# Kernel tuning notes

Measured on AMD Instinct MI355X. Metric: run time of the kernel, lower is better.

Reference implementation:

```python
import jax, jax.numpy as jnp
import numpy as np

NUM_HEADS = 16
HEAD_DIM = 64
HIDDEN = NUM_HEADS * HEAD_DIM
LN_EPS = 1e-6


def setup_inputs() -> dict:
    key = jax.random.key(0)
    ks = jax.random.split(key, 5)
    B, T, H = 2, 2048, HIDDEN
    s = 1.0 / np.sqrt(H)
    return {
        "h": jax.random.normal(ks[0], (B, T, H), jnp.float32),
        "Wq": jax.random.normal(ks[1], (H, H), jnp.float32) * s,
        "bq": jnp.zeros((H,), jnp.float32),
        "Wk": jax.random.normal(ks[2], (H, H), jnp.float32) * s,
        "bk": jnp.zeros((H,), jnp.float32),
        "Wv": jax.random.normal(ks[3], (H, H), jnp.float32) * s,
        "bv": jnp.zeros((H,), jnp.float32),
        "Wo": jax.random.normal(ks[4], (H, H), jnp.float32) * s,
        "bo": jnp.zeros((H,), jnp.float32),
        "gamma": jnp.ones((H,), jnp.float32),
        "beta": jnp.zeros((H,), jnp.float32),
    }


def _split_heads(x):
    B, T, H = x.shape
    return x.reshape(B, T, NUM_HEADS, HEAD_DIM).transpose(0, 2, 1, 3)  # [B,h,T,d]


def reference(h, Wq, bq, Wk, bk, Wv, bv, Wo, bo, gamma, beta):
    # QKV projections (nn.Linear: x @ W^T + b)
    Q = _split_heads(h @ Wq.T + bq)
    K = _split_heads(h @ Wk.T + bk)
    V = _split_heads(h @ Wv.T + bv)
    scale = HEAD_DIM ** -0.5
    scores = jnp.einsum("bhqd,bhkd->bhqk", Q, K) * scale  # [B,h,T,T]
    attn = jax.nn.softmax(scores, axis=-1)
    ctx = jnp.einsum("bhqk,bhkd->bhqd", attn, V)          # [B,h,T,d]
    B, _, T, _ = ctx.shape
    ctx = ctx.transpose(0, 2, 1, 3).reshape(B, T, HIDDEN)
    out = ctx @ Wo.T + bo + h  # dropout is identity at eval
    # LayerNorm(eps=1e-6)
    mu = out.mean(-1, keepdims=True)
    var = jnp.mean((out - mu) ** 2, -1, keepdims=True)
    return (out - mu) * jax.lax.rsqrt(var + LN_EPS) * gamma + beta
```

## Files before the change

### kernel.cpp

```cpp
#include <hip/hip_runtime.h>
#include <hip/hip_bf16.h>

#define NH   16
#define HD   64
#define HID  1024
#define TSEQ 2048
#define BATCH 2
#define KSCALE 0.18033688011112042f

typedef __attribute__((ext_vector_type(4))) float f32x4;
typedef __attribute__((ext_vector_type(8))) short s16x8;
typedef __attribute__((ext_vector_type(4))) short s16x4;
typedef __attribute__((ext_vector_type(8))) _Float16 f16x8;
typedef __attribute__((ext_vector_type(4))) _Float16 f16x4;
typedef __attribute__((ext_vector_type(2))) _Float16 f16x2;

__device__ __forceinline__ unsigned short f2bf(float f) {
  union { float f; unsigned int u; } v; v.f = f;
  unsigned int r = v.u + 0x7fffu + ((v.u >> 16) & 1u);
  return (unsigned short)(r >> 16);
}
__device__ __forceinline__ float bf2f(unsigned short b) {
  union { unsigned int u; float f; } v; v.u = ((unsigned int)b) << 16; return v.f;
}

__device__ __forceinline__ void async_cp16(const unsigned short* g, unsigned short* l) {
  __builtin_amdgcn_global_load_lds(
      (const __attribute__((address_space(1))) unsigned int*)g,
      (__attribute__((address_space(3))) unsigned int*)l, 16, 0, 0);
}

__global__ __launch_bounds__(256) void cast_all_k(
    const float* __restrict__ h,
    const float* __restrict__ w0, const float* __restrict__ w1,
    const float* __restrict__ w2, const float* __restrict__ w3,
    unsigned short* __restrict__ hb, unsigned short* __restrict__ wbase) {
  int i = blockIdx.x * 256 + threadIdx.x;
  const float* src; unsigned short* dst; int idx; float sc = 1.f;
  if (i < 1048576) { src = h; dst = hb; idx = i; }
  else {
    int idx4 = i - 1048576;
    int w = idx4 >> 18;
    idx = idx4 & 262143;
    src = (w == 0) ? w0 : (w == 1) ? w1 : (w == 2) ? w2 : w3;
    dst = wbase + (size_t)(idx4 - idx) * 4;
    if (w == 1) sc = KSCALE;
  }
  float4 v = ((const float4*)src)[idx];
  ushort4 o;
  o.x = f2bf(v.x * sc); o.y = f2bf(v.y * sc); o.z = f2bf(v.z * sc); o.w = f2bf(v.w * sc);
  ((ushort4*)dst)[idx] = o;
}

__global__ __launch_bounds__(256) void gemm_qkv(
    const unsigned short* __restrict__ hb,
    const unsigned short* __restrict__ wq, const unsigned short* __restrict__ wk,
    const unsigned short* __restrict__ wv,
    const float* __restrict__ bq, const float* __restrict__ bk, const float* __restrict__ bv,
    unsigned short* __restrict__ qo, unsigned short* __restrict__ ko,
    unsigned short* __restrict__ vto) {
  __shared__ unsigned short Ash[64 * 32];
  __shared__ unsigned short Bsh[3][64 * 32];
  const int tid = threadIdx.x, lane = tid & 63, wave = tid >> 6;
  const int l15 = lane & 15, quad = lane >> 4;
  const int wn = wave * 16;
  const int bm = blockIdx.y * 64, bn = blockIdx.x * 64;
  const unsigned short* Ag = hb + (size_t)bm * HID;
  const unsigned short* Bg0 = wq + (size_t)bn * HID;
  const unsigned short* Bg1 = wk + (size_t)bn * HID;
  const unsigned short* Bg2 = wv + (size_t)bn * HID;
  const int idx = tid * 8;
  const int rA = idx >> 5, cA = idx & 31;

  f32x4 acc[3][4];
#pragma unroll
  for (int m = 0; m < 3; ++m)
#pragma unroll
    for (int i = 0; i < 4; ++i) acc[m][i] = f32x4{0.f, 0.f, 0.f, 0.f};

  for (int k0 = 0; k0 < HID; k0 += 32) {
    __syncthreads();
    async_cp16(Ag  + rA * HID + k0 + cA, Ash    + idx);
    async_cp16(Bg0 + rA * HID + k0 + cA, Bsh[0] + idx);
    async_cp16(Bg1 + rA * HID + k0 + cA, Bsh[1] + idx);
    async_cp16(Bg2 + rA * HID + k0 + cA, Bsh[2] + idx);
    __syncthreads();
    s16x8 af[4];
#pragma unroll
    for (int i = 0; i < 4; ++i)
      af[i] = *(const s16x8*)(Ash + (i * 16 + l15) * 32 + quad * 8);
#pragma unroll
    for (int m = 0; m < 3; ++m) {
      s16x8 bfr = *(const s16x8*)(Bsh[m] + (wn + l15) * 32 + quad * 8);
#pragma unroll
      for (int i = 0; i < 4; ++i)
        acc[m][i] = __builtin_amdgcn_mfma_f32_16x16x32_bf16(af[i], bfr, acc[m][i], 0, 0, 0);
    }
  }

  const int col = bn + wn + l15;
  const int head = col >> 6, d = col & 63;
  {
    const float bb = bq[col];
#pragma unroll
    for (int i = 0; i < 4; ++i) {
#pragma unroll
      for (int r = 0; r < 4; ++r) {
        const int row = bm + i * 16 + quad * 4 + r;
        const int bI = row >> 11, t = row & 2047;
        qo[(((size_t)(bI * NH + head) * TSEQ) + t) * HD + d] = f2bf(acc[0][i][r] + bb);
      }
    }
  }
  {
    const float bb = bk[col] * KSCALE;
#pragma unroll
    for (int i = 0; i < 4; ++i) {
#pragma unroll
      for (int r = 0; r < 4; ++r) {
        const int row = bm + i * 16 + quad * 4 + r;
        const int bI = row >> 11, t = row & 2047;
        ko[(((size_t)(bI * NH + head) * TSEQ) + t) * HD + d] = f2bf(acc[1][i][r] + bb);
      }
    }
  }
  {
    const float bb = bv[col];
#pragma unroll
    for (int i = 0; i < 4; ++i) {
      const int row0 = bm + i * 16 + quad * 4;
      const int bI = row0 >> 11, t0 = row0 & 2047;
      unsigned short o[4];
#pragma unroll
      for (int r = 0; r < 4; ++r) {
        _Float16 hv = (_Float16)(acc[2][i][r] + bb);
        o[r] = __builtin_bit_cast(unsigned short, hv);
      }
      *(s16x4*)(vto + ((size_t)((bI * NH + head) * HD + d)) * TSEQ + t0) = *(const s16x4*)o;
    }
  }
}

__global__ __launch_bounds__(256) void gemm_out(
    const unsigned short* __restrict__ ctx, const unsigned short* __restrict__ wo,
    const float* __restrict__ bo, const float* __restrict__ hres,
    float* __restrict__ outf) {
  __shared__ unsigned short Ash[128 * 32];
  __shared__ unsigned short Bsh[64 * 32];
  const int tid = threadIdx.x, lane = tid & 63, wave = tid >> 6;
  const int l15 = lane & 15, quad = lane >> 4;
  const int wm = (wave >> 1) * 64, wn = (wave & 1) * 32;
  const int bm = blockIdx.y * 128, bn = blockIdx.x * 64;
  const unsigned short* Ag = ctx + (size_t)bm * HID;
  const unsigned short* Bg = wo + (size_t)bn * HID;
  const int idx0 = tid * 8, idx1 = idx0 + 2048;
  const int r0 = idx0 >> 5, c0 = idx0 & 31;
  const int r1 = idx1 >> 5, c1 = idx1 & 31;
  f32x4 acc[4][2];
#pragma unroll
  for (int i = 0; i < 4; ++i)
#pragma unroll
    for (int j = 0; j < 2; ++j) acc[i][j] = f32x4{0.f, 0.f, 0.f, 0.f};

  for (int k0 = 0; k0 < HID; k0 += 32) {
    __syncthreads();
    async_cp16(Ag + r0 * HID + k0 + c0, Ash + idx0);
    async_cp16(Ag + r1 * HID + k0 + c1, Ash + idx1);
    async_cp16(Bg + r0 * HID + k0 + c0, Bsh + idx0);
    __syncthreads();
    s16x8 af[4], bfr[2];
#pragma unroll
    for (int i = 0; i < 4; ++i)
      af[i] = *(const s16x8*)(Ash + (wm + i * 16 + l15) * 32 + quad * 8);
#pragma unroll
    for (int j = 0; j < 2; ++j)
      bfr[j] = *(const s16x8*)(Bsh + (wn + j * 16 + l15) * 32 + quad * 8);
#pragma unroll
    for (int i = 0; i < 4; ++i)
#pragma unroll
      for (int j = 0; j < 2; ++j)
        acc[i][j] = __builtin_amdgcn_mfma_f32_16x16x32_bf16(af[i], bfr[j], acc[i][j], 0, 0, 0);
  }
#pragma unroll
  for (int j = 0; j < 2; ++j) {
    const int col = bn + wn + j * 16 + l15;
    const float bb = bo[col];
#pragma unroll
    for (int i = 0; i < 4; ++i) {
#pragma unroll
      for (int r = 0; r < 4; ++r) {
        const int row = bm + wm + i * 16 + quad * 4 + r;
        const size_t off = (size_t)row * HID + col;
        outf[off] = acc[i][j][r] + bb + hres[off];
      }
    }
  }
}

__global__ __launch_bounds__(256, 2) void attn_k(
    const unsigned short* __restrict__ qb, const unsigned short* __restrict__ kb,
    const unsigned short* __restrict__ vt, unsigned short* __restrict__ ctx,
    unsigned short* __restrict__ Opart, float* __restrict__ rsumP,
    int lsplit, int ntiles) {
  __shared__ unsigned short Ksh[64 * 72];
  __shared__ unsigned short Vsh[64 * 72];

  const int tid = threadIdx.x, lane = tid & 63, wave = tid >> 6;
  const int l15 = lane & 15, quad = lane >> 4;
  const int z = blockIdx.z;
  const int b = z >> lsplit;
  const int part = z & ((1 << lsplit) - 1);
  const int h = blockIdx.y, qt = blockIdx.x;
  const size_t ho = ((size_t)(b * NH + h)) * TSEQ * HD;
  const unsigned short* Qh = qb + ho;
  const unsigned short* Kh = kb + ho;
  const unsigned short* Vh = vt + ho;
  const int q0 = qt * 128 + wave * 32;
  const int kt0 = part * ntiles;

  s16x8 qf[2][2];
#pragma unroll
  for (int s = 0; s < 2; ++s)
#pragma unroll
    for (int ks = 0; ks < 2; ++ks)
      qf[s][ks] = *(const s16x8*)(Qh + (size_t)(q0 + s * 16 + l15) * HD + ks * 32 + quad * 8);

  f32x4 accO[4][2];
  float rsum[2];
#pragma unroll
  for (int n2 = 0; n2 < 4; ++n2)
#pragma unroll
    for (int s = 0; s < 2; ++s) accO[n2][s] = f32x4{0.f, 0.f, 0.f, 0.f};
  rsum[0] = rsum[1] = 0.f;

  const int sr = tid >> 3, sc = (tid & 7) * 8;
  s16x8 kreg[2], vreg[2];
#pragma unroll
  for (int hf = 0; hf < 2; ++hf) {
    kreg[hf] = *(const s16x8*)(Kh + (size_t)(kt0 * 64 + sr + hf * 32) * HD + sc);
    vreg[hf] = *(const s16x8*)(Vh + (size_t)(sr + hf * 32) * TSEQ + kt0 * 64 + sc);
  }

  for (int kt = 0; kt < ntiles; ++kt) {
    __syncthreads();
#pragma unroll
    for (int hf = 0; hf < 2; ++hf) {
      *(s16x8*)(Ksh + (sr + hf * 32) * 72 + sc) = kreg[hf];
      *(s16x8*)(Vsh + (sr + hf * 32) * 72 + sc) = vreg[hf];
    }
    __syncthreads();
    if (kt + 1 < ntiles) {
      const int k0n = (kt0 + kt + 1) * 64;
#pragma unroll
      for (int hf = 0; hf < 2; ++hf) {
        kreg[hf] = *(const s16x8*)(Kh + (size_t)(k0n + sr + hf * 32) * HD + sc);
        vreg[hf] = *(const s16x8*)(Vh + (size_t)(sr + hf * 32) * TSEQ + k0n + sc);
      }
    }

    f32x4 accS[2][4];
#pragma unroll
    for (int s = 0; s < 2; ++s)
#pragma unroll
      for (int n = 0; n < 4; ++n) accS[s][n] = f32x4{0.f, 0.f, 0.f, 0.f};
#pragma unroll
    for (int ks = 0; ks < 2; ++ks) {
#pragma unroll
      for (int n = 0; n < 4; ++n) {
        s16x8 kf = *(const s16x8*)(Ksh + (n * 16 + l15) * 72 + ks * 32 + quad * 8);
#pragma unroll
        for (int s = 0; s < 2; ++s)
          accS[s][n] = __builtin_amdgcn_mfma_f32_16x16x32_bf16(kf, qf[s][ks], accS[s][n], 0, 0, 0);
      }
    }

    f16x4 pB[2][4];
#pragma unroll
    for (int s = 0; s < 2; ++s)
#pragma unroll
      for (int n = 0; n < 4; ++n) {
        float e0 = __builtin_amdgcn_exp2f(accS[s][n][0]);
        float e1 = __builtin_amdgcn_exp2f(accS[s][n][1]);
        float e2 = __builtin_amdgcn_exp2f(accS[s][n][2]);
        float e3 = __builtin_amdgcn_exp2f(accS[s][n][3]);
        rsum[s] += (e0 + e1) + (e2 + e3);
        f16x2 lo = __builtin_bit_cast(f16x2, __builtin_amdgcn_cvt_pkrtz(e0, e1));
        f16x2 hi = __builtin_bit_cast(f16x2, __builtin_amdgcn_cvt_pkrtz(e2, e3));
        pB[s][n] = f16x4{lo[0], lo[1], hi[0], hi[1]};
      }

#pragma unroll
    for (int n = 0; n < 4; ++n) {
#pragma unroll
      for (int n2 = 0; n2 < 4; ++n2) {
        f16x4 vA = *(const f16x4*)(Vsh + (n2 * 16 + l15) * 72 + n * 16 + quad * 4);
#pragma unroll
        for (int s = 0; s < 2; ++s)
          accO[n2][s] = __builtin_amdgcn_mfma_f32_16x16x16f16(vA, pB[s][n], accO[n2][s], 0, 0, 0);
      }
    }
  }

#pragma unroll
  for (int s = 0; s < 2; ++s) {
    float t = rsum[s];
    t += __shfl_xor(t, 16, 64);
    t += __shfl_xor(t, 32, 64);
    rsum[s] = t;
  }

  if (lsplit) {
    const int slot = (part * BATCH + b) * NH + h;
    const size_t ob = (size_t)slot * TSEQ * HD;
#pragma unroll
    for (int s = 0; s < 2; ++s) {
      const int t = q0 + s * 16 + l15;
#pragma unroll
      for (int n2 = 0; n2 < 4; ++n2) {
        const int d0 = n2 * 16 + quad * 4;
        unsigned short o[4];
#pragma unroll
        for (int r = 0; r < 4; ++r) o[r] = f2bf(accO[n2][s][r]);
        *(s16x4*)(Opart + ob + (size_t)t * HD + d0) = *(const s16x4*)o;
      }
    }
    if (quad == 0) {
      const size_t rb = (size_t)slot * TSEQ;
#pragma unroll
      for (int s = 0; s < 2; ++s)
        rsumP[rb + q0 + s * 16 + l15] = rsum[s];
    }
  } else {
#pragma unroll
    for (int s = 0; s < 2; ++s) {
      const int t = q0 + s * 16 + l15;
      const float inv = 1.f / rsum[s];
#pragma unroll
      for (int n2 = 0; n2 < 4; ++n2) {
        const int d0 = n2 * 16 + quad * 4;
        unsigned short o[4];
#pragma unroll
        for (int r = 0; r < 4; ++r) o[r] = f2bf(accO[n2][s][r] * inv);
        *(s16x4*)(ctx + ((size_t)(b * TSEQ + t)) * HID + h * HD + d0) = *(const s16x4*)o;
      }
    }
  }
}

__global__ __launch_bounds__(256) void combine_k(
    const unsigned short* __restrict__ Opart, const float* __restrict__ rsumP,
    unsigned short* __restrict__ ctx, int nparts) {
  const int gtid = blockIdx.x * 256 + threadIdx.x;
  const int d = (gtid & 7) * 8;
  const int rem = gtid >> 3;
  const int t = rem & 2047;
  const int bh = rem >> 11;
  float acc[8] = {0, 0, 0, 0, 0, 0, 0, 0};
  float rs = 0.f;
  for (int p = 0; p < nparts; ++p) {
    const int slot = p * 32 + bh;
    s16x8 a = *(const s16x8*)(Opart + ((size_t)slot * TSEQ + t) * HD + d);
#pragma unroll
    for (int j = 0; j < 8; ++j) acc[j] += bf2f(((const unsigned short*)&a)[j]);
    rs += rsumP[(size_t)slot * TSEQ + t];
  }
  const float inv = 1.f / rs;
  unsigned short o[8];
#pragma unroll
  for (int j = 0; j < 8; ++j) o[j] = f2bf(acc[j] * inv);
  const int b = bh >> 4, h = bh & 15;
  *(s16x8*)(ctx + ((size_t)(b * TSEQ + t)) * HID + h * HD + d) = *(const s16x8*)o;
}

__global__ __launch_bounds__(256) void ln_k(float* __restrict__ io,
                                            const float* __restrict__ gamma,
                                            const float* __restrict__ beta) {
  const int row = blockIdx.x, tid = threadIdx.x;
  float x[4]; float s = 0.f, s2 = 0.f;
#pragma unroll
  for (int i = 0; i < 4; ++i) {
    x[i] = io[(size_t)row * HID + tid + i * 256];
    s += x[i]; s2 += x[i] * x[i];
  }
#pragma unroll
  for (int off = 1; off < 64; off <<= 1) {
    s  += __shfl_xor(s, off, 64);
    s2 += __shfl_xor(s2, off, 64);
  }
  __shared__ float red[8];
  const int wave = tid >> 6;
  if ((tid & 63) == 0) { red[wave] = s; red[wave + 4] = s2; }
  __syncthreads();
  s  = red[0] + red[1] + red[2] + red[3];
  s2 = red[4] + red[5] + red[6] + red[7];
  const float mean = s * (1.f / HID);
  const float var  = s2 * (1.f / HID) - mean * mean;
  const float rstd = rsqrtf(var + 1e-6f);
#pragma unroll
  for (int i = 0; i < 4; ++i) {
    const int col = tid + i * 256;
    io[(size_t)row * HID + col] = (x[i] - mean) * rstd * gamma[col] + beta[col];
  }
}

extern "C" void kernel_launch(void* const* d_in, const int* in_sizes, int n_in,
                              void* d_out, int out_size, void* d_ws, size_t ws_size,
                              hipStream_t stream) {
  const float* h    = (const float*)d_in[0];
  const float* Wq   = (const float*)d_in[1];
  const float* bq   = (const float*)d_in[2];
  const float* Wk   = (const float*)d_in[3];
  const float* bk   = (const float*)d_in[4];
  const float* Wv   = (const float*)d_in[5];
  const float* bv   = (const float*)d_in[6];
  const float* Wo   = (const float*)d_in[7];
  const float* bo   = (const float*)d_in[8];
  const float* gamma = (const float*)d_in[9];
  const float* beta  = (const float*)d_in[10];
  float* out = (float*)d_out;

  unsigned short* hb   = (unsigned short*)d_ws;
  unsigned short* wqb  = hb  + 4194304;
  unsigned short* wkb  = wqb + 1048576;
  unsigned short* wvb  = wkb + 1048576;
  unsigned short* wob  = wvb + 1048576;
  unsigned short* qb   = wob + 1048576;
  unsigned short* kb   = qb  + 4194304;
  unsigned short* vtf  = kb  + 4194304;
  unsigned short* Opart = vtf + 4194304;
  unsigned short* ctxb = hb;

  const size_t base = (size_t)(vtf + 4194304 - hb) * 2;
  int lsplit = 0;
  if (ws_size >= base + 2u * 8388608 + 2u * 262144) lsplit = 1;
  const int nparts = 1 << lsplit;
  float* rsumP = (float*)(Opart + (size_t)nparts * 4194304);

  cast_all_k<<<8192, 256, 0, stream>>>(h, Wq, Wk, Wv, Wo, hb, wqb);
  gemm_qkv<<<dim3(16, 64), 256, 0, stream>>>(hb, wqb, wkb, wvb, bq, bk, bv, qb, kb, vtf);
  attn_k<<<dim3(TSEQ / 128, NH, BATCH << lsplit), 256, 0, stream>>>(
      qb, kb, vtf, ctxb, Opart, rsumP, lsplit, 32 >> lsplit);
  if (lsplit)
    combine_k<<<2048, 256, 0, stream>>>(Opart, rsumP, ctxb, nparts);
  gemm_out<<<dim3(16, 32), 256, 0, stream>>>(ctxb, wob, bo, h, out);
  ln_k<<<4096, 256, 0, stream>>>(out, gamma, beta);
}
```

Measured before the change: 220.8 us.

## Prefetch next K-tile into registers in QKV and output GEMMs

Replaces the direct global-to-LDS async copies in the QKV projection and output projection GEMMs with register prefetching. The next K-slice is loaded into registers while the current slice is being consumed by MFMAs, then written to LDS at the top of the next iteration. This is meant to hide global load latency behind compute, at the cost of extra registers and explicit LDS store instructions.

```diff
diff --git a/kernel.cpp b/kernel.cpp
--- a/kernel.cpp
+++ b/kernel.cpp
@@ -22,12 +22,6 @@
 }
 __device__ __forceinline__ float bf2f(unsigned short b) {
   union { unsigned int u; float f; } v; v.u = ((unsigned int)b) << 16; return v.f;
-}
-
-__device__ __forceinline__ void async_cp16(const unsigned short* g, unsigned short* l) {
-  __builtin_amdgcn_global_load_lds(
-      (const __attribute__((address_space(1))) unsigned int*)g,
-      (__attribute__((address_space(3))) unsigned int*)l, 16, 0, 0);
 }
 
 __global__ __launch_bounds__(256) void cast_all_k(
@@ -71,6 +65,7 @@
   const unsigned short* Bg2 = wv + (size_t)bn * HID;
   const int idx = tid * 8;
   const int rA = idx >> 5, cA = idx & 31;
+  const size_t goff = (size_t)rA * HID + cA;
 
   f32x4 acc[3][4];
 #pragma unroll
@@ -78,13 +73,25 @@
 #pragma unroll
     for (int i = 0; i < 4; ++i) acc[m][i] = f32x4{0.f, 0.f, 0.f, 0.f};
 
+  s16x8 pa, pb0, pb1, pb2;
+  pa  = *(const s16x8*)(Ag  + goff);
+  pb0 = *(const s16x8*)(Bg0 + goff);
+  pb1 = *(const s16x8*)(Bg1 + goff);
+  pb2 = *(const s16x8*)(Bg2 + goff);
+
   for (int k0 = 0; k0 < HID; k0 += 32) {
     __syncthreads();
-    async_cp16(Ag  + rA * HID + k0 + cA, Ash    + idx);
-    async_cp16(Bg0 + rA * HID + k0 + cA, Bsh[0] + idx);
-    async_cp16(Bg1 + rA * HID + k0 + cA, Bsh[1] + idx);
-    async_cp16(Bg2 + rA * HID + k0 + cA, Bsh[2] + idx);
-    __syncthreads();
+    *(s16x8*)(Ash    + idx) = pa;
+    *(s16x8*)(Bsh[0] + idx) = pb0;
+    *(s16x8*)(Bsh[1] + idx) = pb1;
+    *(s16x8*)(Bsh[2] + idx) = pb2;
+    __syncthreads();
+    if (k0 + 32 < HID) {
+      pa  = *(const s16x8*)(Ag  + goff + k0 + 32);
+      pb0 = *(const s16x8*)(Bg0 + goff + k0 + 32);
+      pb1 = *(const s16x8*)(Bg1 + goff + k0 + 32);
+      pb2 = *(const s16x8*)(Bg2 + goff + k0 + 32);
+    }
     s16x8 af[4];
 #pragma unroll
     for (int i = 0; i < 4; ++i)
@@ -156,18 +163,28 @@
   const int idx0 = tid * 8, idx1 = idx0 + 2048;
   const int r0 = idx0 >> 5, c0 = idx0 & 31;
   const int r1 = idx1 >> 5, c1 = idx1 & 31;
+  const size_t g0 = (size_t)r0 * HID + c0, g1 = (size_t)r1 * HID + c1;
   f32x4 acc[4][2];
 #pragma unroll
   for (int i = 0; i < 4; ++i)
 #pragma unroll
     for (int j = 0; j < 2; ++j) acc[i][j] = f32x4{0.f, 0.f, 0.f, 0.f};
 
+  s16x8 pa0 = *(const s16x8*)(Ag + g0);
+  s16x8 pa1 = *(const s16x8*)(Ag + g1);
+  s16x8 pb  = *(const s16x8*)(Bg + g0);
+
   for (int k0 = 0; k0 < HID; k0 += 32) {
     __syncthreads();
-    async_cp16(Ag + r0 * HID + k0 + c0, Ash + idx0);
-    async_cp16(Ag + r1 * HID + k0 + c1, Ash + idx1);
-    async_cp16(Bg + r0 * HID + k0 + c0, Bsh + idx0);
-    __syncthreads();
+    *(s16x8*)(Ash + idx0) = pa0;
+    *(s16x8*)(Ash + idx1) = pa1;
+    *(s16x8*)(Bsh + idx0) = pb;
+    __syncthreads();
+    if (k0 + 32 < HID) {
+      pa0 = *(const s16x8*)(Ag + g0 + k0 + 32);
+      pa1 = *(const s16x8*)(Ag + g1 + k0 + 32);
+      pb  = *(const s16x8*)(Bg + g0 + k0 + 32);
+    }
     s16x8 af[4], bfr[2];
 #pragma unroll
     for (int i = 0; i < 4; ++i)
```

Result: no change. 219.5 us (-0.6%).

## Prefetch GEMM tiles into registers two steps ahead instead of direct-to-LDS loads

Applied to the files above, without the earlier changes.

Both the QKV projection GEMM and the output GEMM stop using global_load_lds async copies. They now keep a two-stage register prefetch buffer: global loads for k-step k+2 are issued before the MFMAs of step k, and the staged registers are written to LDS at the start of each step. This hides global memory latency behind compute instead of stalling on the barrier after each copy. The cost is extra VGPRs and an explicit LDS store pass.

```diff
diff --git a/kernel.cpp b/kernel.cpp
--- a/kernel.cpp
+++ b/kernel.cpp
@@ -11,7 +11,6 @@
 typedef __attribute__((ext_vector_type(4))) float f32x4;
 typedef __attribute__((ext_vector_type(8))) short s16x8;
 typedef __attribute__((ext_vector_type(4))) short s16x4;
-typedef __attribute__((ext_vector_type(8))) _Float16 f16x8;
 typedef __attribute__((ext_vector_type(4))) _Float16 f16x4;
 typedef __attribute__((ext_vector_type(2))) _Float16 f16x2;
 
@@ -22,12 +21,6 @@
 }
 __device__ __forceinline__ float bf2f(unsigned short b) {
   union { unsigned int u; float f; } v; v.u = ((unsigned int)b) << 16; return v.f;
-}
-
-__device__ __forceinline__ void async_cp16(const unsigned short* g, unsigned short* l) {
-  __builtin_amdgcn_global_load_lds(
-      (const __attribute__((address_space(1))) unsigned int*)g,
-      (__attribute__((address_space(3))) unsigned int*)l, 16, 0, 0);
 }
 
 __global__ __launch_bounds__(256) void cast_all_k(
@@ -71,6 +64,7 @@
   const unsigned short* Bg2 = wv + (size_t)bn * HID;
   const int idx = tid * 8;
   const int rA = idx >> 5, cA = idx & 31;
+  const size_t goff = (size_t)rA * HID + cA;
 
   f32x4 acc[3][4];
 #pragma unroll
@@ -78,13 +72,32 @@
 #pragma unroll
     for (int i = 0; i < 4; ++i) acc[m][i] = f32x4{0.f, 0.f, 0.f, 0.f};
 
+  s16x8 pa[2], pb0[2], pb1[2], pb2[2];
+#pragma unroll
+  for (int st = 0; st < 2; ++st) {
+    const size_t o = goff + st * 32;
+    pa[st]  = *(const s16x8*)(Ag  + o);
+    pb0[st] = *(const s16x8*)(Bg0 + o);
+    pb1[st] = *(const s16x8*)(Bg1 + o);
+    pb2[st] = *(const s16x8*)(Bg2 + o);
+  }
+
+#pragma unroll 2
   for (int k0 = 0; k0 < HID; k0 += 32) {
-    __syncthreads();
-    async_cp16(Ag  + rA * HID + k0 + cA, Ash    + idx);
-    async_cp16(Bg0 + rA * HID + k0 + cA, Bsh[0] + idx);
-    async_cp16(Bg1 + rA * HID + k0 + cA, Bsh[1] + idx);
-    async_cp16(Bg2 + rA * HID + k0 + cA, Bsh[2] + idx);
-    __syncthreads();
+    const int st = (k0 >> 5) & 1;
+    __syncthreads();
+    *(s16x8*)(Ash    + idx) = pa[st];
+    *(s16x8*)(Bsh[0] + idx) = pb0[st];
+    *(s16x8*)(Bsh[1] + idx) = pb1[st];
+    *(s16x8*)(Bsh[2] + idx) = pb2[st];
+    __syncthreads();
+    if (k0 + 64 < HID) {
+      const size_t o = goff + k0 + 64;
+      pa[st]  = *(const s16x8*)(Ag  + o);
+      pb0[st] = *(const s16x8*)(Bg0 + o);
+      pb1[st] = *(const s16x8*)(Bg1 + o);
+      pb2[st] = *(const s16x8*)(Bg2 + o);
+    }
     s16x8 af[4];
 #pragma unroll
     for (int i = 0; i < 4; ++i)
@@ -156,18 +169,34 @@
   const int idx0 = tid * 8, idx1 = idx0 + 2048;
   const int r0 = idx0 >> 5, c0 = idx0 & 31;
   const int r1 = idx1 >> 5, c1 = idx1 & 31;
+  const size_t g0 = (size_t)r0 * HID + c0, g1 = (size_t)r1 * HID + c1;
   f32x4 acc[4][2];
 #pragma unroll
   for (int i = 0; i < 4; ++i)
 #pragma unroll
     for (int j = 0; j < 2; ++j) acc[i][j] = f32x4{0.f, 0.f, 0.f, 0.f};
 
+  s16x8 pa0[2], pa1[2], pb[2];
+#pragma unroll
+  for (int st = 0; st < 2; ++st) {
+    pa0[st] = *(const s16x8*)(Ag + g0 + st * 32);
+    pa1[st] = *(const s16x8*)(Ag + g1 + st * 32);
+    pb[st]  = *(const s16x8*)(Bg + g0 + st * 32);
+  }
+
+#pragma unroll 2
   for (int k0 = 0; k0 < HID; k0 += 32) {
-    __syncthreads();
-    async_cp16(Ag + r0 * HID + k0 + c0, Ash + idx0);
-    async_cp16(Ag + r1 * HID + k0 + c1, Ash + idx1);
-    async_cp16(Bg + r0 * HID + k0 + c0, Bsh + idx0);
-    __syncthreads();
+    const int st = (k0 >> 5) & 1;
+    __syncthreads();
+    *(s16x8*)(Ash + idx0) = pa0[st];
+    *(s16x8*)(Ash + idx1) = pa1[st];
+    *(s16x8*)(Bsh + idx0) = pb[st];
+    __syncthreads();
+    if (k0 + 64 < HID) {
+      pa0[st] = *(const s16x8*)(Ag + g0 + k0 + 64);
+      pa1[st] = *(const s16x8*)(Ag + g1 + k0 + 64);
+      pb[st]  = *(const s16x8*)(Bg + g0 + k0 + 64);
+    }
     s16x8 af[4], bfr[2];
 #pragma unroll
     for (int i = 0; i < 4; ++i)
```

After: 225.0 us. About the same (+1.9%).
